# Kernel optimization log

Measured on AMD Instinct MI355X. Metric: run time of the kernel, lower is better.

The kernel has to match this reference:

```python
import jax, jax.numpy as jnp
import numpy as np

COMMITMENT_COST = 0.25


def setup_inputs() -> dict:
    key = jax.random.key(0)
    k1, k2 = jax.random.split(key)
    inputs = jax.random.normal(k1, (64, 4096, 64), dtype=jnp.float32)
    codewords = jax.random.normal(k2, (512, 64), dtype=jnp.float32)
    return {"inputs": inputs, "codewords": codewords}


def reference(inputs, codewords):
    D = codewords.shape[-1]
    flat = inputs.reshape(-1, D)  # (N, D)
    # squared Euclidean distances (N, K) via expansion, avoiding the (N, K, D) tensor
    x_sq = jnp.sum(flat * flat, axis=-1, keepdims=True)          # (N, 1)
    c_sq = jnp.sum(codewords * codewords, axis=-1)               # (K,)
    distances = x_sq - 2.0 * (flat @ codewords.T) + c_sq         # (N, K)
    encoding_indices = jnp.argmin(distances, axis=1)             # (N,)
    quantized = jnp.take(codewords, encoding_indices, axis=0).reshape(inputs.shape)
    commitment_loss = jnp.mean((jax.lax.stop_gradient(quantized) - inputs) ** 2)
    loss = COMMITMENT_COST * commitment_loss
    encoding_indices = encoding_indices.reshape(inputs.shape[:-1])
    return quantized, encoding_indices, loss
```

## Files before the change

### kernel.cpp

```cpp
#include <hip/hip_runtime.h>


typedef _Float16 half8 __attribute__((ext_vector_type(8)));
typedef float    floatx4 __attribute__((ext_vector_type(4)));

#define NVEC  262144
#define DDIM  64
#define KCW   512
#define LOSS_SCALE (0.25f / 16777216.0f)
#define DMARGIN 0.005f
#define BROWS 512
#define NBLK  (NVEC / BROWS)

#define SM_BS     0
#define SM_CSQH   139264
#define SM_WIN    141312
#define SM_LIST   143360
#define SM_FLG    145408
#define SM_RED    145920
#define SM_CNT    145952
#define SMEM_BYTES 146176

#define WS_CSQ   0
#define WS_CSQH  2048
#define WS_HL    8192

__global__ void prep_kernel(const float* __restrict__ cw,
                            float* __restrict__ csq,
                            float* __restrict__ csqh,
                            _Float16* __restrict__ cw_hl,
                            float* __restrict__ loss_slot) {
    int n = blockIdx.x * blockDim.x + threadIdx.x;
    if (n < KCW) {
        const float4* r = (const float4*)(cw + n * DDIM);
        _Float16* orow = cw_hl + n * 128;
        float s = 0.f;
        #pragma unroll
        for (int t = 0; t < 8; ++t) {
            float4 a = r[2 * t], b = r[2 * t + 1];
            half8 hh, ll;
            #pragma unroll
            for (int i = 0; i < 4; ++i) {
                float v = ((const float*)&a)[i];
                s += v * v;
                _Float16 h = (_Float16)v;
                hh[i] = h; ll[i] = (_Float16)(v - (float)h);
                v = ((const float*)&b)[i];
                s += v * v;
                h = (_Float16)v;
                hh[4 + i] = h; ll[4 + i] = (_Float16)(v - (float)h);
            }
            *(half8*)(orow + 8 * t) = hh;
            *(half8*)(orow + 64 + 8 * t) = ll;
        }
        csq[n]  = s;
        csqh[n] = 0.5f * s;
    }
    if (n == 0) *loss_slot = 0.f;
}

__global__ __launch_bounds__(512, 2)
void vq_mfma_kernel(const float* __restrict__ x,
                    const float* __restrict__ cw,
                    const _Float16* __restrict__ cw_hl,
                    const float* __restrict__ csqh,
                    const float* __restrict__ csq,
                    float* __restrict__ out_q,
                    float* __restrict__ out_idx,
                    float* __restrict__ out_loss) {
    extern __shared__ char smem[];
    _Float16*      Bs     = (_Float16*)(smem + SM_BS);
    float*         csqhs  = (float*)(smem + SM_CSQH);
    int*           win    = (int*)(smem + SM_WIN);
    int*           lslist = (int*)(smem + SM_LIST);
    unsigned char* flg    = (unsigned char*)(smem + SM_FLG);
    float*         red    = (float*)(smem + SM_RED);
    unsigned*      lcnt   = (unsigned*)(smem + SM_CNT);

    const int tid  = threadIdx.x;
    const int w    = tid >> 6;
    const int lane = tid & 63;
    const int quad = lane >> 4;
    const int col  = lane & 15;
    const int blk  = blockIdx.x * BROWS;

    if (tid == 0) *lcnt = 0u;
    csqhs[tid] = -csqh[tid];

    {
        const half8* g = (const half8*)cw_hl;
        #pragma unroll
        for (int k = 0; k < 16; ++k) {
            int c = k * 512 + tid;
            *(half8*)(Bs + (c >> 4) * 136 + (c & 15) * 8) = g[c];
        }
    }

    half8 ah0[4], ah1[4], al0[4], al1[4];
    #pragma unroll
    for (int rt = 0; rt < 4; ++rt) {
        const float* xr = x + (size_t)(blk + w * 64 + rt * 16 + col) * DDIM;
        float4 f0 = *(const float4*)(xr + quad * 8);
        float4 f1 = *(const float4*)(xr + quad * 8 + 4);
        float4 g0 = *(const float4*)(xr + 32 + quad * 8);
        float4 g1 = *(const float4*)(xr + 32 + quad * 8 + 4);
        #pragma unroll
        for (int i = 0; i < 4; ++i) {
            float v = ((const float*)&f0)[i];
            _Float16 h = (_Float16)v;
            ah0[rt][i] = h; al0[rt][i] = (_Float16)(v - (float)h);
            v = ((const float*)&f1)[i]; h = (_Float16)v;
            ah0[rt][4 + i] = h; al0[rt][4 + i] = (_Float16)(v - (float)h);
            v = ((const float*)&g0)[i]; h = (_Float16)v;
            ah1[rt][i] = h; al1[rt][i] = (_Float16)(v - (float)h);
            v = ((const float*)&g1)[i]; h = (_Float16)v;
            ah1[rt][4 + i] = h; al1[rt][4 + i] = (_Float16)(v - (float)h);
        }
    }

    float M1[16], M2[16];
    int   idx[16];
    #pragma unroll
    for (int s = 0; s < 16; ++s) {
        M1[s] = -3.402823466e38f; M2[s] = -3.402823466e38f; idx[s] = 0;
    }

    __syncthreads();

    #pragma unroll 2
    for (int t = 0; t < 32; ++t) {
        const int n  = t * 16 + col;
        const int nb = n * 136;
        half8 bh0 = *(const half8*)&Bs[nb + quad * 8];
        half8 bh1 = *(const half8*)&Bs[nb + 32 + quad * 8];
        half8 bl0 = *(const half8*)&Bs[nb + 64 + quad * 8];
        half8 bl1 = *(const half8*)&Bs[nb + 96 + quad * 8];
        const float vn = csqhs[n];

        #pragma unroll
        for (int rt = 0; rt < 4; ++rt) {
            floatx4 acc = {vn, vn, vn, vn};
            acc = __builtin_amdgcn_mfma_f32_16x16x32_f16(ah0[rt], bh0, acc, 0, 0, 0);
            acc = __builtin_amdgcn_mfma_f32_16x16x32_f16(ah1[rt], bh1, acc, 0, 0, 0);
            acc = __builtin_amdgcn_mfma_f32_16x16x32_f16(al0[rt], bh0, acc, 0, 0, 0);
            acc = __builtin_amdgcn_mfma_f32_16x16x32_f16(al1[rt], bh1, acc, 0, 0, 0);
            acc = __builtin_amdgcn_mfma_f32_16x16x32_f16(ah0[rt], bl0, acc, 0, 0, 0);
            acc = __builtin_amdgcn_mfma_f32_16x16x32_f16(ah1[rt], bl1, acc, 0, 0, 0);
            #pragma unroll
            for (int reg = 0; reg < 4; ++reg) {
                int s = rt * 4 + reg;
                float d = acc[reg];
                if (d > M1[s]) idx[s] = n;
                M2[s] = __builtin_amdgcn_fmed3f(M1[s], M2[s], d);
                M1[s] = fmaxf(M1[s], d);
            }
        }
    }

    #pragma unroll
    for (int off = 1; off < 16; off <<= 1) {
        #pragma unroll
        for (int s = 0; s < 16; ++s) {
            float o1 = __shfl_xor(M1[s], off, 16);
            float o2 = __shfl_xor(M2[s], off, 16);
            int   oi = __shfl_xor(idx[s], off, 16);
            float mn = fminf(M1[s], o1);
            M2[s] = fmaxf(fmaxf(M2[s], o2), mn);
            if (o1 > M1[s] || (o1 == M1[s] && oi < idx[s])) idx[s] = oi;
            M1[s] = fmaxf(M1[s], o1);
        }
    }

    if (col < 4) {
        #pragma unroll
        for (int rt = 0; rt < 4; ++rt) {
            int s  = rt * 4 + col;
            int rl = w * 64 + rt * 16 + quad * 4 + col;
            int nw = idx[s];
            int f  = (M1[s] - M2[s] <= DMARGIN) ? 1 : 0;
            win[rl] = nw;
            flg[rl] = (unsigned char)f;
            out_idx[blk + rl] = (float)nw;
            if (f) { unsigned p = atomicAdd(lcnt, 1u); lslist[p] = rl; }
        }
    }
    __syncthreads();

    float ls = 0.f;
    #pragma unroll
    for (int k = 0; k < 16; ++k) {
        int rl = k * 32 + (tid >> 4);
        int e4 = (tid & 15) * 4;
        int wn = win[rl];
        int f  = flg[rl];
        float4 q  = *(const float4*)(cw + wn * DDIM + e4);
        float4 xv = *(const float4*)(x + (size_t)(blk + rl) * DDIM + e4);
        *(float4*)(out_q + (size_t)(blk + rl) * DDIM + e4) = q;
        if (!f) {
            float d0 = q.x - xv.x, d1 = q.y - xv.y;
            float d2 = q.z - xv.z, d3 = q.w - xv.w;
            ls += d0 * d0 + d1 * d1 + d2 * d2 + d3 * d3;
        }
    }
    #pragma unroll
    for (int off = 32; off > 0; off >>= 1) ls += __shfl_down(ls, off, 64);
    if (lane == 0) red[w] = ls;
    __syncthreads();
    if (tid == 0) {
        float s = 0.f;
        #pragma unroll
        for (int i = 0; i < 8; ++i) s += red[i];
        atomicAdd(out_loss, s * LOSS_SCALE);
    }

    const unsigned cnt = *lcnt;
    const int grp = tid >> 4;
    const int tx  = tid & 15;
    for (unsigned i = (unsigned)grp; i < cnt; i += 32) {
        const int rl = lslist[i];
        const size_t row = (size_t)blk + rl;

        float4 xr[16];
        const float4* xg = (const float4*)(x + row * DDIM);
        #pragma unroll
        for (int t = 0; t < 16; ++t) xr[t] = xg[t];

        float best = 3.402823466e38f; int bi = 0;
        for (int j = 0; j < 32; ++j) {
            int n = tx + 16 * j;
            const float4* c = (const float4*)(cw + n * DDIM);
            float a0 = 0.f, a1 = 0.f, a2 = 0.f, a3 = 0.f;
            #pragma unroll
            for (int t = 0; t < 16; ++t) {
                float4 cv = c[t];
                a0 = __builtin_fmaf(xr[t].x, cv.x, a0);
                a1 = __builtin_fmaf(xr[t].y, cv.y, a1);
                a2 = __builtin_fmaf(xr[t].z, cv.z, a2);
                a3 = __builtin_fmaf(xr[t].w, cv.w, a3);
            }
            float sc = __builtin_fmaf(-2.f, (a0 + a1) + (a2 + a3), csq[n]);
            if (sc < best) { best = sc; bi = n; }
        }
        #pragma unroll
        for (int off = 8; off > 0; off >>= 1) {
            float d2 = __shfl_down(best, off, 16);
            int   i2 = __shfl_down(bi,   off, 16);
            if (d2 < best || (d2 == best && i2 < bi)) { best = d2; bi = i2; }
        }
        if (tx == 0) {
            out_idx[row] = (float)bi;
            const float4* qg = (const float4*)(cw + bi * DDIM);
            float4* og = (float4*)(out_q + row * DDIM);
            float lf = 0.f;
            #pragma unroll
            for (int t = 0; t < 16; ++t) {
                float4 q = qg[t];
                og[t] = q;
                float d0 = q.x - xr[t].x, d1 = q.y - xr[t].y;
                float d2_ = q.z - xr[t].z, d3 = q.w - xr[t].w;
                lf += d0 * d0 + d1 * d1 + d2_ * d2_ + d3 * d3;
            }
            atomicAdd(out_loss, lf * LOSS_SCALE);
        }
    }
}

extern "C" void kernel_launch(void* const* d_in, const int* in_sizes, int n_in,
                              void* d_out, int out_size, void* d_ws, size_t ws_size,
                              hipStream_t stream) {
    const float* x  = (const float*)d_in[0];
    const float* cw = (const float*)d_in[1];
    float* out      = (float*)d_out;
    float* out_q    = out;
    float* out_idx  = out + 16777216;
    float* out_loss = out + 16777216 + 262144;

    char* ws = (char*)d_ws;
    float*    csq   = (float*)(ws + WS_CSQ);
    float*    csqh  = (float*)(ws + WS_CSQH);
    _Float16* cw_hl = (_Float16*)(ws + WS_HL);

    (void)hipFuncSetAttribute((const void*)vq_mfma_kernel,
                              hipFuncAttributeMaxDynamicSharedMemorySize,
                              SMEM_BYTES);

    prep_kernel<<<8, 64, 0, stream>>>(cw, csq, csqh, cw_hl, out_loss);
    vq_mfma_kernel<<<NBLK, 512, SMEM_BYTES, stream>>>(x, cw, cw_hl, csqh, csq,
                                                      out_q, out_idx, out_loss);
}
```

Baseline: 239.4 us.

## Halve block rows and stream codebook in two LDS chunks for higher occupancy

Each block now handles 256 rows instead of 512 and loads the codebook into shared memory in two 256-entry chunks. The fp16 hi/lo split of the codebook moves from the prep kernel into each block. This halves shared memory per block and per-thread register arrays so launch bounds can request 4 blocks per CU instead of 2, aiming for better latency hiding. The cost is twice as many blocks redundantly converting the codebook from fp32, plus extra barriers between chunks.

```diff
diff --git a/kernel.cpp b/kernel.cpp
--- a/kernel.cpp
+++ b/kernel.cpp
@@ -9,49 +9,34 @@
 #define KCW   512
 #define LOSS_SCALE (0.25f / 16777216.0f)
 #define DMARGIN 0.005f
-#define BROWS 512
+#define BROWS 256
 #define NBLK  (NVEC / BROWS)
+#define CHUNK 256
 
 #define SM_BS     0
-#define SM_CSQH   139264
-#define SM_WIN    141312
-#define SM_LIST   143360
-#define SM_FLG    145408
-#define SM_RED    145920
-#define SM_CNT    145952
-#define SMEM_BYTES 146176
+#define SM_CSQH   69632
+#define SM_WIN    71680
+#define SM_LIST   72704
+#define SM_FLG    73728
+#define SM_RED    73984
+#define SM_CNT    74016
+#define SMEM_BYTES 74112
 
 #define WS_CSQ   0
 #define WS_CSQH  2048
-#define WS_HL    8192
 
 __global__ void prep_kernel(const float* __restrict__ cw,
                             float* __restrict__ csq,
                             float* __restrict__ csqh,
-                            _Float16* __restrict__ cw_hl,
                             float* __restrict__ loss_slot) {
     int n = blockIdx.x * blockDim.x + threadIdx.x;
     if (n < KCW) {
         const float4* r = (const float4*)(cw + n * DDIM);
-        _Float16* orow = cw_hl + n * 128;
         float s = 0.f;
         #pragma unroll
-        for (int t = 0; t < 8; ++t) {
-            float4 a = r[2 * t], b = r[2 * t + 1];
-            half8 hh, ll;
-            #pragma unroll
-            for (int i = 0; i < 4; ++i) {
-                float v = ((const float*)&a)[i];
-                s += v * v;
-                _Float16 h = (_Float16)v;
-                hh[i] = h; ll[i] = (_Float16)(v - (float)h);
-                v = ((const float*)&b)[i];
-                s += v * v;
-                h = (_Float16)v;
-                hh[4 + i] = h; ll[4 + i] = (_Float16)(v - (float)h);
-            }
-            *(half8*)(orow + 8 * t) = hh;
-            *(half8*)(orow + 64 + 8 * t) = ll;
+        for (int t = 0; t < 16; ++t) {
+            float4 a = r[t];
+            s += a.x * a.x + a.y * a.y + a.z * a.z + a.w * a.w;
         }
         csq[n]  = s;
         csqh[n] = 0.5f * s;
@@ -59,10 +44,9 @@
     if (n == 0) *loss_slot = 0.f;
 }
 
-__global__ __launch_bounds__(512, 2)
+__global__ __launch_bounds__(512, 4)
 void vq_mfma_kernel(const float* __restrict__ x,
                     const float* __restrict__ cw,
-                    const _Float16* __restrict__ cw_hl,
                     const float* __restrict__ csqh,
                     const float* __restrict__ csq,
                     float* __restrict__ out_q,
@@ -87,19 +71,10 @@
     if (tid == 0) *lcnt = 0u;
     csqhs[tid] = -csqh[tid];
 
-    {
-        const half8* g = (const half8*)cw_hl;
-        #pragma unroll
-        for (int k = 0; k < 16; ++k) {
-            int c = k * 512 + tid;
-            *(half8*)(Bs + (c >> 4) * 136 + (c & 15) * 8) = g[c];
-        }
-    }
-
-    half8 ah0[4], ah1[4], al0[4], al1[4];
-    #pragma unroll
-    for (int rt = 0; rt < 4; ++rt) {
-        const float* xr = x + (size_t)(blk + w * 64 + rt * 16 + col) * DDIM;
+    half8 ah0[2], ah1[2], al0[2], al1[2];
+    #pragma unroll
+    for (int rt = 0; rt < 2; ++rt) {
+        const float* xr = x + (size_t)(blk + w * 32 + rt * 16 + col) * DDIM;
         float4 f0 = *(const float4*)(xr + quad * 8);
         float4 f1 = *(const float4*)(xr + quad * 8 + 4);
         float4 g0 = *(const float4*)(xr + 32 + quad * 8);
@@ -118,41 +93,66 @@
         }
     }
 
-    float M1[16], M2[16];
-    int   idx[16];
-    #pragma unroll
-    for (int s = 0; s < 16; ++s) {
+    float M1[8], M2[8];
+    int   idx[8];
+    #pragma unroll
+    for (int s = 0; s < 8; ++s) {
         M1[s] = -3.402823466e38f; M2[s] = -3.402823466e38f; idx[s] = 0;
     }
 
-    __syncthreads();
-
-    #pragma unroll 2
-    for (int t = 0; t < 32; ++t) {
-        const int n  = t * 16 + col;
-        const int nb = n * 136;
-        half8 bh0 = *(const half8*)&Bs[nb + quad * 8];
-        half8 bh1 = *(const half8*)&Bs[nb + 32 + quad * 8];
-        half8 bl0 = *(const half8*)&Bs[nb + 64 + quad * 8];
-        half8 bl1 = *(const half8*)&Bs[nb + 96 + quad * 8];
-        const float vn = csqhs[n];
-
-        #pragma unroll
-        for (int rt = 0; rt < 4; ++rt) {
-            floatx4 acc = {vn, vn, vn, vn};
-            acc = __builtin_amdgcn_mfma_f32_16x16x32_f16(ah0[rt], bh0, acc, 0, 0, 0);
-            acc = __builtin_amdgcn_mfma_f32_16x16x32_f16(ah1[rt], bh1, acc, 0, 0, 0);
-            acc = __builtin_amdgcn_mfma_f32_16x16x32_f16(al0[rt], bh0, acc, 0, 0, 0);
-            acc = __builtin_amdgcn_mfma_f32_16x16x32_f16(al1[rt], bh1, acc, 0, 0, 0);
-            acc = __builtin_amdgcn_mfma_f32_16x16x32_f16(ah0[rt], bl0, acc, 0, 0, 0);
-            acc = __builtin_amdgcn_mfma_f32_16x16x32_f16(ah1[rt], bl1, acc, 0, 0, 0);
-            #pragma unroll
-            for (int reg = 0; reg < 4; ++reg) {
-                int s = rt * 4 + reg;
-                float d = acc[reg];
-                if (d > M1[s]) idx[s] = n;
-                M2[s] = __builtin_amdgcn_fmed3f(M1[s], M2[s], d);
-                M1[s] = fmaxf(M1[s], d);
+    for (int ch = 0; ch < 2; ++ch) {
+        __syncthreads();
+        {
+            const int cidx = tid >> 1;
+            const int hh   = tid & 1;
+            const float4* src =
+                (const float4*)(cw + (size_t)(ch * CHUNK + cidx) * DDIM + hh * 32);
+            _Float16* dst = Bs + cidx * 136 + hh * 32;
+            #pragma unroll
+            for (int t = 0; t < 4; ++t) {
+                float4 a = src[2 * t], b = src[2 * t + 1];
+                half8 hv, lv;
+                #pragma unroll
+                for (int i = 0; i < 4; ++i) {
+                    float v = ((const float*)&a)[i];
+                    _Float16 h = (_Float16)v;
+                    hv[i] = h; lv[i] = (_Float16)(v - (float)h);
+                    v = ((const float*)&b)[i]; h = (_Float16)v;
+                    hv[4 + i] = h; lv[4 + i] = (_Float16)(v - (float)h);
+                }
+                *(half8*)(dst + 8 * t) = hv;
+                *(half8*)(dst + 64 + 8 * t) = lv;
+            }
+        }
+        __syncthreads();
+
+        #pragma unroll 2
+        for (int t = 0; t < 16; ++t) {
+            const int n  = ch * CHUNK + t * 16 + col;
+            const int nb = (t * 16 + col) * 136;
+            half8 bh0 = *(const half8*)&Bs[nb + quad * 8];
+            half8 bh1 = *(const half8*)&Bs[nb + 32 + quad * 8];
+            half8 bl0 = *(const half8*)&Bs[nb + 64 + quad * 8];
+            half8 bl1 = *(const half8*)&Bs[nb + 96 + quad * 8];
+            const float vn = csqhs[n];
+
+            #pragma unroll
+            for (int rt = 0; rt < 2; ++rt) {
+                floatx4 acc = {vn, vn, vn, vn};
+                acc = __builtin_amdgcn_mfma_f32_16x16x32_f16(ah0[rt], bh0, acc, 0, 0, 0);
+                acc = __builtin_amdgcn_mfma_f32_16x16x32_f16(ah1[rt], bh1, acc, 0, 0, 0);
+                acc = __builtin_amdgcn_mfma_f32_16x16x32_f16(al0[rt], bh0, acc, 0, 0, 0);
+                acc = __builtin_amdgcn_mfma_f32_16x16x32_f16(al1[rt], bh1, acc, 0, 0, 0);
+                acc = __builtin_amdgcn_mfma_f32_16x16x32_f16(ah0[rt], bl0, acc, 0, 0, 0);
+                acc = __builtin_amdgcn_mfma_f32_16x16x32_f16(ah1[rt], bl1, acc, 0, 0, 0);
+                #pragma unroll
+                for (int reg = 0; reg < 4; ++reg) {
+                    int s = rt * 4 + reg;
+                    float d = acc[reg];
+                    if (d > M1[s]) idx[s] = n;
+                    M2[s] = __builtin_amdgcn_fmed3f(M1[s], M2[s], d);
+                    M1[s] = fmaxf(M1[s], d);
+                }
             }
         }
     }
@@ -160,7 +160,7 @@
     #pragma unroll
     for (int off = 1; off < 16; off <<= 1) {
         #pragma unroll
-        for (int s = 0; s < 16; ++s) {
+        for (int s = 0; s < 8; ++s) {
             float o1 = __shfl_xor(M1[s], off, 16);
             float o2 = __shfl_xor(M2[s], off, 16);
             int   oi = __shfl_xor(idx[s], off, 16);
@@ -173,9 +173,9 @@
 
     if (col < 4) {
         #pragma unroll
-        for (int rt = 0; rt < 4; ++rt) {
+        for (int rt = 0; rt < 2; ++rt) {
             int s  = rt * 4 + col;
-            int rl = w * 64 + rt * 16 + quad * 4 + col;
+            int rl = w * 32 + rt * 16 + quad * 4 + col;
             int nw = idx[s];
             int f  = (M1[s] - M2[s] <= DMARGIN) ? 1 : 0;
             win[rl] = nw;
@@ -188,7 +188,7 @@
 
     float ls = 0.f;
     #pragma unroll
-    for (int k = 0; k < 16; ++k) {
+    for (int k = 0; k < 8; ++k) {
         int rl = k * 32 + (tid >> 4);
         int e4 = (tid & 15) * 4;
         int wn = win[rl];
@@ -276,15 +276,14 @@
     float* out_loss = out + 16777216 + 262144;
 
     char* ws = (char*)d_ws;
-    float*    csq   = (float*)(ws + WS_CSQ);
-    float*    csqh  = (float*)(ws + WS_CSQH);
-    _Float16* cw_hl = (_Float16*)(ws + WS_HL);
+    float* csq  = (float*)(ws + WS_CSQ);
+    float* csqh = (float*)(ws + WS_CSQH);
 
     (void)hipFuncSetAttribute((const void*)vq_mfma_kernel,
                               hipFuncAttributeMaxDynamicSharedMemorySize,
                               SMEM_BYTES);
 
-    prep_kernel<<<8, 64, 0, stream>>>(cw, csq, csqh, cw_hl, out_loss);
-    vq_mfma_kernel<<<NBLK, 512, SMEM_BYTES, stream>>>(x, cw, cw_hl, csqh, csq,
+    prep_kernel<<<8, 64, 0, stream>>>(cw, csq, csqh, out_loss);
+    vq_mfma_kernel<<<NBLK, 512, SMEM_BYTES, stream>>>(x, cw, csqh, csq,
                                                       out_q, out_idx, out_loss);
 }
```

Result: no change. 239.7 us (+0.1%).

## Stream codebook in 64-entry LDS chunks with smaller blocks for higher occupancy

Applied to the files above, without the earlier changes.

Replaces the full 136KB LDS-resident codebook with 64-codeword chunks streamed through a small static LDS buffer. Block size drops to 256 threads and 128 rows, with launch bounds raised to 6 blocks per CU. The MFMA chain is also split into two independent accumulators so consecutive MFMAs can overlap. This is meant to raise occupancy and hide latency, at the cost of 8 extra barrier pairs per block and codebook reloads from L2 for every block.

```diff
diff --git a/kernel.cpp b/kernel.cpp
--- a/kernel.cpp
+++ b/kernel.cpp
@@ -9,17 +9,9 @@
 #define KCW   512
 #define LOSS_SCALE (0.25f / 16777216.0f)
 #define DMARGIN 0.005f
-#define BROWS 512
+#define BROWS 128
 #define NBLK  (NVEC / BROWS)
-
-#define SM_BS     0
-#define SM_CSQH   139264
-#define SM_WIN    141312
-#define SM_LIST   143360
-#define SM_FLG    145408
-#define SM_RED    145920
-#define SM_CNT    145952
-#define SMEM_BYTES 146176
+#define CHUNK 64
 
 #define WS_CSQ   0
 #define WS_CSQH  2048
@@ -59,7 +51,7 @@
     if (n == 0) *loss_slot = 0.f;
 }
 
-__global__ __launch_bounds__(512, 2)
+__global__ __launch_bounds__(256, 6)
 void vq_mfma_kernel(const float* __restrict__ x,
                     const float* __restrict__ cw,
                     const _Float16* __restrict__ cw_hl,
@@ -68,14 +60,13 @@
                     float* __restrict__ out_q,
                     float* __restrict__ out_idx,
                     float* __restrict__ out_loss) {
-    extern __shared__ char smem[];
-    _Float16*      Bs     = (_Float16*)(smem + SM_BS);
-    float*         csqhs  = (float*)(smem + SM_CSQH);
-    int*           win    = (int*)(smem + SM_WIN);
-    int*           lslist = (int*)(smem + SM_LIST);
-    unsigned char* flg    = (unsigned char*)(smem + SM_FLG);
-    float*         red    = (float*)(smem + SM_RED);
-    unsigned*      lcnt   = (unsigned*)(smem + SM_CNT);
+    __shared__ _Float16      Bs[CHUNK * 136];
+    __shared__ float         csqhs[KCW];
+    __shared__ int           win[BROWS];
+    __shared__ int           lslist[BROWS];
+    __shared__ unsigned char flg[BROWS];
+    __shared__ float         red[4];
+    __shared__ unsigned      lcnt;
 
     const int tid  = threadIdx.x;
     const int w    = tid >> 6;
@@ -84,22 +75,14 @@
     const int col  = lane & 15;
     const int blk  = blockIdx.x * BROWS;
 
-    if (tid == 0) *lcnt = 0u;
-    csqhs[tid] = -csqh[tid];
-
-    {
-        const half8* g = (const half8*)cw_hl;
-        #pragma unroll
-        for (int k = 0; k < 16; ++k) {
-            int c = k * 512 + tid;
-            *(half8*)(Bs + (c >> 4) * 136 + (c & 15) * 8) = g[c];
-        }
-    }
-
-    half8 ah0[4], ah1[4], al0[4], al1[4];
-    #pragma unroll
-    for (int rt = 0; rt < 4; ++rt) {
-        const float* xr = x + (size_t)(blk + w * 64 + rt * 16 + col) * DDIM;
+    if (tid == 0) lcnt = 0u;
+    csqhs[tid]       = -csqh[tid];
+    csqhs[tid + 256] = -csqh[tid + 256];
+
+    half8 ah0[2], ah1[2], al0[2], al1[2];
+    #pragma unroll
+    for (int rt = 0; rt < 2; ++rt) {
+        const float* xr = x + (size_t)(blk + w * 32 + rt * 16 + col) * DDIM;
         float4 f0 = *(const float4*)(xr + quad * 8);
         float4 f1 = *(const float4*)(xr + quad * 8 + 4);
         float4 g0 = *(const float4*)(xr + 32 + quad * 8);
@@ -118,41 +101,54 @@
         }
     }
 
-    float M1[16], M2[16];
-    int   idx[16];
-    #pragma unroll
-    for (int s = 0; s < 16; ++s) {
+    float M1[8], M2[8];
+    int   idx[8];
+    #pragma unroll
+    for (int s = 0; s < 8; ++s) {
         M1[s] = -3.402823466e38f; M2[s] = -3.402823466e38f; idx[s] = 0;
     }
 
-    __syncthreads();
-
-    #pragma unroll 2
-    for (int t = 0; t < 32; ++t) {
-        const int n  = t * 16 + col;
-        const int nb = n * 136;
-        half8 bh0 = *(const half8*)&Bs[nb + quad * 8];
-        half8 bh1 = *(const half8*)&Bs[nb + 32 + quad * 8];
-        half8 bl0 = *(const half8*)&Bs[nb + 64 + quad * 8];
-        half8 bl1 = *(const half8*)&Bs[nb + 96 + quad * 8];
-        const float vn = csqhs[n];
-
-        #pragma unroll
-        for (int rt = 0; rt < 4; ++rt) {
-            floatx4 acc = {vn, vn, vn, vn};
-            acc = __builtin_amdgcn_mfma_f32_16x16x32_f16(ah0[rt], bh0, acc, 0, 0, 0);
-            acc = __builtin_amdgcn_mfma_f32_16x16x32_f16(ah1[rt], bh1, acc, 0, 0, 0);
-            acc = __builtin_amdgcn_mfma_f32_16x16x32_f16(al0[rt], bh0, acc, 0, 0, 0);
-            acc = __builtin_amdgcn_mfma_f32_16x16x32_f16(al1[rt], bh1, acc, 0, 0, 0);
-            acc = __builtin_amdgcn_mfma_f32_16x16x32_f16(ah0[rt], bl0, acc, 0, 0, 0);
-            acc = __builtin_amdgcn_mfma_f32_16x16x32_f16(ah1[rt], bl1, acc, 0, 0, 0);
-            #pragma unroll
-            for (int reg = 0; reg < 4; ++reg) {
-                int s = rt * 4 + reg;
-                float d = acc[reg];
-                if (d > M1[s]) idx[s] = n;
-                M2[s] = __builtin_amdgcn_fmed3f(M1[s], M2[s], d);
-                M1[s] = fmaxf(M1[s], d);
+    for (int ch = 0; ch < 8; ++ch) {
+        __syncthreads();
+        {
+            const int cidx = tid >> 2;
+            const int seg  = tid & 3;
+            const half8* src =
+                (const half8*)(cw_hl + ((size_t)(ch * CHUNK + cidx) << 7) + seg * 32);
+            half8* dst = (half8*)(Bs + cidx * 136 + seg * 32);
+            #pragma unroll
+            for (int b = 0; b < 4; ++b) dst[b] = src[b];
+        }
+        __syncthreads();
+
+        #pragma unroll
+        for (int t = 0; t < 4; ++t) {
+            const int n  = ch * CHUNK + t * 16 + col;
+            const int nb = (t * 16 + col) * 136;
+            half8 bh0 = *(const half8*)&Bs[nb + quad * 8];
+            half8 bh1 = *(const half8*)&Bs[nb + 32 + quad * 8];
+            half8 bl0 = *(const half8*)&Bs[nb + 64 + quad * 8];
+            half8 bl1 = *(const half8*)&Bs[nb + 96 + quad * 8];
+            const float vn = csqhs[n];
+
+            #pragma unroll
+            for (int rt = 0; rt < 2; ++rt) {
+                floatx4 accA = {vn, vn, vn, vn};
+                floatx4 accB = {0.f, 0.f, 0.f, 0.f};
+                accA = __builtin_amdgcn_mfma_f32_16x16x32_f16(ah0[rt], bh0, accA, 0, 0, 0);
+                accB = __builtin_amdgcn_mfma_f32_16x16x32_f16(al0[rt], bh0, accB, 0, 0, 0);
+                accA = __builtin_amdgcn_mfma_f32_16x16x32_f16(ah1[rt], bh1, accA, 0, 0, 0);
+                accB = __builtin_amdgcn_mfma_f32_16x16x32_f16(al1[rt], bh1, accB, 0, 0, 0);
+                accA = __builtin_amdgcn_mfma_f32_16x16x32_f16(ah0[rt], bl0, accA, 0, 0, 0);
+                accB = __builtin_amdgcn_mfma_f32_16x16x32_f16(ah1[rt], bl1, accB, 0, 0, 0);
+                #pragma unroll
+                for (int reg = 0; reg < 4; ++reg) {
+                    int s = rt * 4 + reg;
+                    float d = accA[reg] + accB[reg];
+                    if (d > M1[s]) idx[s] = n;
+                    M2[s] = __builtin_amdgcn_fmed3f(M1[s], M2[s], d);
+                    M1[s] = fmaxf(M1[s], d);
+                }
             }
         }
     }
@@ -160,7 +156,7 @@
     #pragma unroll
     for (int off = 1; off < 16; off <<= 1) {
         #pragma unroll
-        for (int s = 0; s < 16; ++s) {
+        for (int s = 0; s < 8; ++s) {
             float o1 = __shfl_xor(M1[s], off, 16);
             float o2 = __shfl_xor(M2[s], off, 16);
             int   oi = __shfl_xor(idx[s], off, 16);
@@ -173,23 +169,23 @@
 
     if (col < 4) {
         #pragma unroll
-        for (int rt = 0; rt < 4; ++rt) {
+        for (int rt = 0; rt < 2; ++rt) {
             int s  = rt * 4 + col;
-            int rl = w * 64 + rt * 16 + quad * 4 + col;
+            int rl = w * 32 + rt * 16 + quad * 4 + col;
             int nw = idx[s];
             int f  = (M1[s] - M2[s] <= DMARGIN) ? 1 : 0;
             win[rl] = nw;
             flg[rl] = (unsigned char)f;
             out_idx[blk + rl] = (float)nw;
-            if (f) { unsigned p = atomicAdd(lcnt, 1u); lslist[p] = rl; }
+            if (f) { unsigned p = atomicAdd(&lcnt, 1u); lslist[p] = rl; }
         }
     }
     __syncthreads();
 
     float ls = 0.f;
     #pragma unroll
-    for (int k = 0; k < 16; ++k) {
-        int rl = k * 32 + (tid >> 4);
+    for (int k = 0; k < 8; ++k) {
+        int rl = k * 16 + (tid >> 4);
         int e4 = (tid & 15) * 4;
         int wn = win[rl];
         int f  = flg[rl];
@@ -206,17 +202,13 @@
     for (int off = 32; off > 0; off >>= 1) ls += __shfl_down(ls, off, 64);
     if (lane == 0) red[w] = ls;
     __syncthreads();
-    if (tid == 0) {
-        float s = 0.f;
-        #pragma unroll
-        for (int i = 0; i < 8; ++i) s += red[i];
-        atomicAdd(out_loss, s * LOSS_SCALE);
-    }
-
-    const unsigned cnt = *lcnt;
+    if (tid == 0)
+        atomicAdd(out_loss, ((red[0] + red[1]) + (red[2] + red[3])) * LOSS_SCALE);
+
+    const unsigned cnt = lcnt;
     const int grp = tid >> 4;
     const int tx  = tid & 15;
-    for (unsigned i = (unsigned)grp; i < cnt; i += 32) {
+    for (unsigned i = (unsigned)grp; i < cnt; i += 16) {
         const int rl = lslist[i];
         const size_t row = (size_t)blk + rl;
 
@@ -280,11 +272,7 @@
     float*    csqh  = (float*)(ws + WS_CSQH);
     _Float16* cw_hl = (_Float16*)(ws + WS_HL);
 
-    (void)hipFuncSetAttribute((const void*)vq_mfma_kernel,
-                              hipFuncAttributeMaxDynamicSharedMemorySize,
-                              SMEM_BYTES);
-
-    prep_kernel<<<8, 64, 0, stream>>>(cw, csq, csqh, cw_hl, out_loss);
-    vq_mfma_kernel<<<NBLK, 512, SMEM_BYTES, stream>>>(x, cw, cw_hl, csqh, csq,
-                                                      out_q, out_idx, out_loss);
+    prep_kernel<<<2, 256, 0, stream>>>(cw, csq, csqh, cw_hl, out_loss);
+    vq_mfma_kernel<<<NBLK, 256, 0, stream>>>(x, cw, cw_hl, csqh, csq,
+                                             out_q, out_idx, out_loss);
 }
```

Result: slower. 756.8 us (+216.2%).
